# Optimization experiments

Measured on AMD Instinct MI355X. Metric: run time of the kernel, lower is better.

## Reference

```python
import jax, jax.numpy as jnp
import numpy as np

S = 5          # sample_num (fixed in source)
N = 400000     # number of splits along dim 2

def setup_inputs() -> dict:
    key = jax.random.key(0)
    k1, k2 = jax.random.split(key)
    out_matrix = jax.random.normal(k1, (S, S, N), dtype=jnp.float32)
    label_matrix = jax.random.normal(k2, (S, S, N), dtype=jnp.float32)
    return {
        "out_matrix": out_matrix,
        "label_matrix": label_matrix,
        "margin": 1,
        "sample_num": S,
    }

def reference(out_matrix, label_matrix, margin, sample_num):
    # Move split dim to front: [N, S, S]
    o = jnp.moveaxis(out_matrix, 2, 0)
    l = jnp.moveaxis(label_matrix, 2, 0)
    margin = jnp.asarray(margin, dtype=o.dtype)

    # Per split n, per row i: loss_matrix[j,k] = (o[n,i,j]-o[n,i,k]) * (l[n,i,j]-l[n,i,k])
    t1 = o[:, :, :, None] - o[:, :, None, :]   # [N, S, S, S]
    t2 = l[:, :, :, None] - l[:, :, None, :]   # [N, S, S, S]
    loss = jnp.sum(jax.nn.relu(margin - t1 * t2))

    # flat_accuracy per split: row-wise argmax agreement, summed over all splits
    pred_max = jnp.argmax(o, axis=2)    # [N, S]
    label_max = jnp.argmax(l, axis=2)   # [N, S]
    correction_num = jnp.sum(pred_max == label_max)

    return (loss, correction_num)
```

## Files before the change

kernel.cpp:

```cpp
#include <hip/hip_runtime.h>

#define SAMPLE_S 5

__global__ void init_out_kernel(float* out) {
    if (threadIdx.x == 0) {
        out[0] = 0.0f;
        out[1] = 0.0f;
    }
}

__device__ __forceinline__ float f4_get(const float4& v, int c) {
    switch (c) {
        case 0: return v.x;
        case 1: return v.y;
        case 2: return v.z;
        default: return v.w;
    }
}

__device__ __forceinline__ void process_row(const float ox[SAMPLE_S], const float lx[SAMPLE_S],
                                            float margin, float& loss, float& cnt) {
    int po = 0, pl = 0;
    float mo = ox[0], ml = lx[0];
#pragma unroll
    for (int j = 1; j < SAMPLE_S; ++j) {
        bool bo = ox[j] > mo;
        mo = bo ? ox[j] : mo;
        po = bo ? j : po;
        bool bl = lx[j] > ml;
        ml = bl ? lx[j] : ml;
        pl = bl ? j : pl;
    }
    if (po == pl) cnt += 1.0f;

    loss += fmaxf(margin, 0.0f) * (float)SAMPLE_S;
#pragma unroll
    for (int j = 0; j < SAMPLE_S; ++j) {
#pragma unroll
        for (int k = j + 1; k < SAMPLE_S; ++k) {
            float t = margin - (ox[j] - ox[k]) * (lx[j] - lx[k]);
            loss += 2.0f * fmaxf(t, 0.0f);
        }
    }
}

__global__ __launch_bounds__(256) void pml_main_kernel(
        const float* __restrict__ o, const float* __restrict__ l,
        const int* __restrict__ margin_p, float* __restrict__ out, int N) {
    const float margin = (float)(*margin_p);
    const long long t  = (long long)blockIdx.x * 256 + threadIdx.x;
    const long long n4 = t * 4;

    float loss = 0.0f, cnt = 0.0f;

    if (n4 + 3 < (long long)N) {
#pragma unroll
        for (int i = 0; i < SAMPLE_S; ++i) {
            float4 ov[SAMPLE_S], lv[SAMPLE_S];
#pragma unroll
            for (int j = 0; j < SAMPLE_S; ++j) {
                const long long base = (long long)(i * SAMPLE_S + j) * N + n4;
                ov[j] = *reinterpret_cast<const float4*>(o + base);
                lv[j] = *reinterpret_cast<const float4*>(l + base);
            }
#pragma unroll
            for (int c = 0; c < 4; ++c) {
                float ox[SAMPLE_S], lx[SAMPLE_S];
#pragma unroll
                for (int j = 0; j < SAMPLE_S; ++j) {
                    ox[j] = f4_get(ov[j], c);
                    lx[j] = f4_get(lv[j], c);
                }
                process_row(ox, lx, margin, loss, cnt);
            }
        }
    } else if (n4 < (long long)N) {
        for (long long n = n4; n < (long long)N; ++n) {
#pragma unroll
            for (int i = 0; i < SAMPLE_S; ++i) {
                float ox[SAMPLE_S], lx[SAMPLE_S];
#pragma unroll
                for (int j = 0; j < SAMPLE_S; ++j) {
                    const long long idx = (long long)(i * SAMPLE_S + j) * N + n;
                    ox[j] = o[idx];
                    lx[j] = l[idx];
                }
                process_row(ox, lx, margin, loss, cnt);
            }
        }
    }

#pragma unroll
    for (int off = 32; off > 0; off >>= 1) {
        loss += __shfl_down(loss, off, 64);
        cnt  += __shfl_down(cnt,  off, 64);
    }
    __shared__ float sl[4], sc[4];
    const int wave = threadIdx.x >> 6;
    const int lane = threadIdx.x & 63;
    if (lane == 0) { sl[wave] = loss; sc[wave] = cnt; }
    __syncthreads();
    if (threadIdx.x == 0) {
        float L = sl[0] + sl[1] + sl[2] + sl[3];
        float C = sc[0] + sc[1] + sc[2] + sc[3];
        atomicAdd(&out[0], L);
        atomicAdd(&out[1], C);
    }
}

extern "C" void kernel_launch(void* const* d_in, const int* in_sizes, int n_in,
                              void* d_out, int out_size, void* d_ws, size_t ws_size,
                              hipStream_t stream) {
    const float* o      = (const float*)d_in[0];
    const float* l      = (const float*)d_in[1];
    const int*   margin = (const int*)d_in[2];
    float*       out    = (float*)d_out;

    const int N = in_sizes[0] / (SAMPLE_S * SAMPLE_S);

    hipLaunchKernelGGL(init_out_kernel, dim3(1), dim3(64), 0, stream, out);

    const long long threads = ((long long)N + 3) / 4;
    const int blocks = (int)((threads + 255) / 256);
    hipLaunchKernelGGL(pml_main_kernel, dim3(blocks), dim3(256), 0, stream,
                       o, l, margin, out, N);
}
```

Before: 108.1 us.

## Use fixed persistent grid with per-block partials and a separate reduce kernel

Drops the init kernel and the per-block global atomics. The main kernel now runs on a fixed grid of 512 blocks that grid-stride over contiguous chunk ranges, writes per-block partial sums to workspace, and a single-block kernel reduces them deterministically. Fewer blocks means less atomic contention and launch overhead, but with ~100k float4 chunks over 512x256 threads, occupancy may be lower than the original ~391-block one-shot grid and latency hiding could suffer.

New measurement: 105.2 us. 2.7% less time.

```diff
diff --git a/kernel.cpp b/kernel.cpp
--- a/kernel.cpp
+++ b/kernel.cpp
@@ -1,13 +1,8 @@
 #include <hip/hip_runtime.h>
 
 #define SAMPLE_S 5
-
-__global__ void init_out_kernel(float* out) {
-    if (threadIdx.x == 0) {
-        out[0] = 0.0f;
-        out[1] = 0.0f;
-    }
-}
+#define NBLOCKS  512
+#define TPB      256
 
 __device__ __forceinline__ float f4_get(const float4& v, int c) {
     switch (c) {
@@ -44,16 +39,22 @@
     }
 }
 
-__global__ __launch_bounds__(256) void pml_main_kernel(
+__global__ __launch_bounds__(TPB) void pml_main_kernel(
         const float* __restrict__ o, const float* __restrict__ l,
-        const int* __restrict__ margin_p, float* __restrict__ out, int N) {
+        const int* __restrict__ margin_p, float* __restrict__ ws, int N) {
     const float margin = (float)(*margin_p);
-    const long long t  = (long long)blockIdx.x * 256 + threadIdx.x;
-    const long long n4 = t * 4;
+    const int b = blockIdx.x;
+    const int t = threadIdx.x;
+
+    const int C = N >> 2;
+    const int q = C / NBLOCKS, r = C % NBLOCKS;
+    const int cstart = b * q + (b < r ? b : r);
+    const int cend   = cstart + q + (b < r ? 1 : 0);
 
     float loss = 0.0f, cnt = 0.0f;
 
-    if (n4 + 3 < (long long)N) {
+    for (int c = cstart + t; c < cend; c += TPB) {
+        const long long n4 = (long long)c << 2;
 #pragma unroll
         for (int i = 0; i < SAMPLE_S; ++i) {
             float4 ov[SAMPLE_S], lv[SAMPLE_S];
@@ -64,29 +65,31 @@
                 lv[j] = *reinterpret_cast<const float4*>(l + base);
             }
 #pragma unroll
-            for (int c = 0; c < 4; ++c) {
+            for (int cc = 0; cc < 4; ++cc) {
                 float ox[SAMPLE_S], lx[SAMPLE_S];
 #pragma unroll
                 for (int j = 0; j < SAMPLE_S; ++j) {
-                    ox[j] = f4_get(ov[j], c);
-                    lx[j] = f4_get(lv[j], c);
+                    ox[j] = f4_get(ov[j], cc);
+                    lx[j] = f4_get(lv[j], cc);
                 }
                 process_row(ox, lx, margin, loss, cnt);
             }
         }
-    } else if (n4 < (long long)N) {
-        for (long long n = n4; n < (long long)N; ++n) {
+    }
+
+    const int r4 = N & 3;
+    if (b == 0 && t < r4) {
+        const long long n = ((long long)C << 2) + t;
 #pragma unroll
-            for (int i = 0; i < SAMPLE_S; ++i) {
-                float ox[SAMPLE_S], lx[SAMPLE_S];
+        for (int i = 0; i < SAMPLE_S; ++i) {
+            float ox[SAMPLE_S], lx[SAMPLE_S];
 #pragma unroll
-                for (int j = 0; j < SAMPLE_S; ++j) {
-                    const long long idx = (long long)(i * SAMPLE_S + j) * N + n;
-                    ox[j] = o[idx];
-                    lx[j] = l[idx];
-                }
-                process_row(ox, lx, margin, loss, cnt);
+            for (int j = 0; j < SAMPLE_S; ++j) {
+                const long long idx = (long long)(i * SAMPLE_S + j) * N + n;
+                ox[j] = o[idx];
+                lx[j] = l[idx];
             }
+            process_row(ox, lx, margin, loss, cnt);
         }
     }
 
@@ -95,16 +98,41 @@
         loss += __shfl_down(loss, off, 64);
         cnt  += __shfl_down(cnt,  off, 64);
     }
-    __shared__ float sl[4], sc[4];
-    const int wave = threadIdx.x >> 6;
-    const int lane = threadIdx.x & 63;
+    __shared__ float sl[TPB / 64], sc[TPB / 64];
+    const int wave = t >> 6;
+    const int lane = t & 63;
     if (lane == 0) { sl[wave] = loss; sc[wave] = cnt; }
     __syncthreads();
-    if (threadIdx.x == 0) {
-        float L = sl[0] + sl[1] + sl[2] + sl[3];
-        float C = sc[0] + sc[1] + sc[2] + sc[3];
-        atomicAdd(&out[0], L);
-        atomicAdd(&out[1], C);
+    if (t == 0) {
+        float L = 0.0f, Cc = 0.0f;
+#pragma unroll
+        for (int w = 0; w < TPB / 64; ++w) { L += sl[w]; Cc += sc[w]; }
+        ws[b]           = L;
+        ws[NBLOCKS + b] = Cc;
+    }
+}
+
+__global__ __launch_bounds__(NBLOCKS) void pml_reduce_kernel(
+        const float* __restrict__ ws, float* __restrict__ out) {
+    const int t = threadIdx.x;
+    float loss = ws[t];
+    float cnt  = ws[NBLOCKS + t];
+#pragma unroll
+    for (int off = 32; off > 0; off >>= 1) {
+        loss += __shfl_down(loss, off, 64);
+        cnt  += __shfl_down(cnt,  off, 64);
+    }
+    __shared__ float sl[NBLOCKS / 64], sc[NBLOCKS / 64];
+    const int wave = t >> 6;
+    const int lane = t & 63;
+    if (lane == 0) { sl[wave] = loss; sc[wave] = cnt; }
+    __syncthreads();
+    if (t == 0) {
+        float L = 0.0f, Cc = 0.0f;
+#pragma unroll
+        for (int w = 0; w < NBLOCKS / 64; ++w) { L += sl[w]; Cc += sc[w]; }
+        out[0] = L;
+        out[1] = Cc;
     }
 }
 
@@ -115,13 +143,12 @@
     const float* l      = (const float*)d_in[1];
     const int*   margin = (const int*)d_in[2];
     float*       out    = (float*)d_out;
+    float*       ws     = (float*)d_ws;
 
     const int N = in_sizes[0] / (SAMPLE_S * SAMPLE_S);
 
-    hipLaunchKernelGGL(init_out_kernel, dim3(1), dim3(64), 0, stream, out);
-
-    const long long threads = ((long long)N + 3) / 4;
-    const int blocks = (int)((threads + 255) / 256);
-    hipLaunchKernelGGL(pml_main_kernel, dim3(blocks), dim3(256), 0, stream,
-                       o, l, margin, out, N);
+    hipLaunchKernelGGL(pml_main_kernel, dim3(NBLOCKS), dim3(TPB), 0, stream,
+                       o, l, margin, ws, N);
+    hipLaunchKernelGGL(pml_reduce_kernel, dim3(1), dim3(NBLOCKS), 0, stream,
+                       ws, out);
 }
```
